# Kernel tuning notes

Measured on AMD Instinct MI355X. Metric: run time of the kernel, lower is better.

The kernel has to match this reference:

```python
import jax, jax.numpy as jnp
import numpy as np

BATCH, SEQ, CHANNELS, KSIZE = 4, 4096, 2048, 4


def setup_inputs() -> dict:
    key = jax.random.key(0)
    kx, kw = jax.random.split(key)
    x = jax.random.normal(kx, (BATCH, SEQ, CHANNELS), dtype=jnp.float32)
    # flax param init: normal(stddev=0.02), shape (kernel_size, channels)
    kernel = jax.random.normal(kw, (KSIZE, CHANNELS), dtype=jnp.float32) * 0.02
    return {"x": x, "kernel": kernel}


def reference(x, kernel):
    # Causal depthwise short conv: y[:, t] = silu(sum_j kernel[j] * x[:, t - j])
    # (the scan's window * kernel[::-1] unrolls to exactly this), with zero
    # left-padding of K-1 steps standing in for cache=None -> zeros.
    B, T, C = x.shape
    K = kernel.shape[0]
    kf = kernel.astype(x.dtype)
    cache = jnp.zeros((B, K - 1, C), dtype=x.dtype)
    xp = jnp.concatenate([cache, x], axis=1)  # [B, T+K-1, C]
    # Small fixed loop over kernel taps (K=4), fully parallel over time.
    y = kf[0][None, None, :] * xp[:, K - 1 : K - 1 + T, :]
    for j in range(1, K):
        y = y + kf[j][None, None, :] * xp[:, K - 1 - j : K - 1 - j + T, :]
    y = jax.nn.silu(y)
    # next_cache after the scan = last K-1 inputs of the padded stream
    next_cache = xp[:, T:, :]  # [B, K-1, C]
    return y, next_cache
```

## Files before the change

kernel.cpp:

```cpp
#include <hip/hip_runtime.h>
#include <math.h>


#define B_   4
#define T_   4096
#define C_   2048
#define K_   4
#define C4_  (C_ / 4)
#define TT_  32

__global__ __launch_bounds__(C4_) void dwconv_silu_kernel(
    const float4* __restrict__ x,
    const float4* __restrict__ kern,
    float4* __restrict__ y)
{
    const int c4 = threadIdx.x;
    const int b  = blockIdx.y;
    const int t0 = blockIdx.x * TT_;

    const float4 k0 = kern[0 * C4_ + c4];
    const float4 k1 = kern[1 * C4_ + c4];
    const float4 k2 = kern[2 * C4_ + c4];
    const float4 k3 = kern[3 * C4_ + c4];

    const float4* xb = x + (size_t)b * T_ * C4_;
    float4*       yb = y + (size_t)b * T_ * C4_;

    float4 xm1, xm2, xm3;
    if (t0 == 0) {
        xm1 = make_float4(0.f, 0.f, 0.f, 0.f);
        xm2 = xm1;
        xm3 = xm1;
    } else {
        xm1 = xb[(size_t)(t0 - 1) * C4_ + c4];
        xm2 = xb[(size_t)(t0 - 2) * C4_ + c4];
        xm3 = xb[(size_t)(t0 - 3) * C4_ + c4];
    }

    #pragma unroll 4
    for (int i = 0; i < TT_; ++i) {
        const int t = t0 + i;
        const float4 x0 = xb[(size_t)t * C4_ + c4];

        float4 r;
        r.x = fmaf(k0.x, x0.x, fmaf(k1.x, xm1.x, fmaf(k2.x, xm2.x, k3.x * xm3.x)));
        r.y = fmaf(k0.y, x0.y, fmaf(k1.y, xm1.y, fmaf(k2.y, xm2.y, k3.y * xm3.y)));
        r.z = fmaf(k0.z, x0.z, fmaf(k1.z, xm1.z, fmaf(k2.z, xm2.z, k3.z * xm3.z)));
        r.w = fmaf(k0.w, x0.w, fmaf(k1.w, xm1.w, fmaf(k2.w, xm2.w, k3.w * xm3.w)));

        r.x = r.x / (1.f + expf(-r.x));
        r.y = r.y / (1.f + expf(-r.y));
        r.z = r.z / (1.f + expf(-r.z));
        r.w = r.w / (1.f + expf(-r.w));

        yb[(size_t)t * C4_ + c4] = r;

        xm3 = xm2;
        xm2 = xm1;
        xm1 = x0;
    }
}

__global__ __launch_bounds__(256) void cache_copy_kernel(
    const float4* __restrict__ x, float4* __restrict__ cache)
{
    const int i = blockIdx.x * blockDim.x + threadIdx.x;
    if (i >= B_ * (K_ - 1) * C4_) return;
    const int b  = i / ((K_ - 1) * C4_);
    const int rc = i % ((K_ - 1) * C4_);
    const int t  = T_ - (K_ - 1) + rc / C4_;
    const int c4 = rc % C4_;
    cache[i] = x[((size_t)b * T_ + t) * C4_ + c4];
}

extern "C" void kernel_launch(void* const* d_in, const int* in_sizes, int n_in,
                              void* d_out, int out_size, void* d_ws, size_t ws_size,
                              hipStream_t stream)
{
    const float4* x    = (const float4*)d_in[0];
    const float4* kern = (const float4*)d_in[1];
    float*        out  = (float*)d_out;

    float4* y     = (float4*)out;
    float4* cache = (float4*)(out + (size_t)B_ * T_ * C_);

    dim3 grid(T_ / TT_, B_);
    dim3 block(C4_);
    dwconv_silu_kernel<<<grid, block, 0, stream>>>(x, kern, y);

    const int cache_elems4 = B_ * (K_ - 1) * C4_;
    cache_copy_kernel<<<(cache_elems4 + 255) / 256, 256, 0, stream>>>(x, cache);
}
```

Before: 242.6 us.

## Unroll conv loop with batched loads, nontemporal stores, fast SiLU, smaller time tile

Halves the per-block time tile, which doubles the block count and adds more halo re-reads. The time loop is fully unrolled so four consecutive rows are loaded together before computing. Output is written with nontemporal stores to avoid polluting cache, and SiLU now uses fast __expf plus a reciprocal instead of a divide. An occupancy hint of 8 blocks per CU is also added to the launch bounds. The intent is more memory-level parallelism for a bandwidth-bound kernel, at a small cost in accuracy from the fast math.

```diff
diff --git a/kernel.cpp b/kernel.cpp
--- a/kernel.cpp
+++ b/kernel.cpp
@@ -7,9 +7,20 @@
 #define C_   2048
 #define K_   4
 #define C4_  (C_ / 4)
-#define TT_  32
+#define TT_  16
 
-__global__ __launch_bounds__(C4_) void dwconv_silu_kernel(
+typedef float nat_float4 __attribute__((ext_vector_type(4)));
+
+__device__ __forceinline__ float silu_f(float v) {
+    return v * __frcp_rn(1.f + __expf(-v));
+}
+
+__device__ __forceinline__ void store_nt(float4* p, const float4& v) {
+    nat_float4 nv = { v.x, v.y, v.z, v.w };
+    __builtin_nontemporal_store(nv, reinterpret_cast<nat_float4*>(p));
+}
+
+__global__ __launch_bounds__(C4_, 8) void dwconv_silu_kernel(
     const float4* __restrict__ x,
     const float4* __restrict__ kern,
     float4* __restrict__ y)
@@ -23,8 +34,8 @@
     const float4 k2 = kern[2 * C4_ + c4];
     const float4 k3 = kern[3 * C4_ + c4];
 
-    const float4* xb = x + (size_t)b * T_ * C4_;
-    float4*       yb = y + (size_t)b * T_ * C4_;
+    const float4* xb = x + (size_t)b * T_ * C4_ + c4;
+    float4*       yb = y + (size_t)b * T_ * C4_ + c4;
 
     float4 xm1, xm2, xm3;
     if (t0 == 0) {
@@ -32,33 +43,41 @@
         xm2 = xm1;
         xm3 = xm1;
     } else {
-        xm1 = xb[(size_t)(t0 - 1) * C4_ + c4];
-        xm2 = xb[(size_t)(t0 - 2) * C4_ + c4];
-        xm3 = xb[(size_t)(t0 - 3) * C4_ + c4];
+        xm1 = xb[(size_t)(t0 - 1) * C4_];
+        xm2 = xb[(size_t)(t0 - 2) * C4_];
+        xm3 = xb[(size_t)(t0 - 3) * C4_];
     }
 
-    #pragma unroll 4
-    for (int i = 0; i < TT_; ++i) {
-        const int t = t0 + i;
-        const float4 x0 = xb[(size_t)t * C4_ + c4];
+#define CONV1(r, a, w1, w2, w3)                                              \
+    r.x = fmaf(k0.x, a.x, fmaf(k1.x, w1.x, fmaf(k2.x, w2.x, k3.x * w3.x)));  \
+    r.y = fmaf(k0.y, a.y, fmaf(k1.y, w1.y, fmaf(k2.y, w2.y, k3.y * w3.y)));  \
+    r.z = fmaf(k0.z, a.z, fmaf(k1.z, w1.z, fmaf(k2.z, w2.z, k3.z * w3.z)));  \
+    r.w = fmaf(k0.w, a.w, fmaf(k1.w, w1.w, fmaf(k2.w, w2.w, k3.w * w3.w)));  \
+    r.x = silu_f(r.x); r.y = silu_f(r.y); r.z = silu_f(r.z); r.w = silu_f(r.w);
 
-        float4 r;
-        r.x = fmaf(k0.x, x0.x, fmaf(k1.x, xm1.x, fmaf(k2.x, xm2.x, k3.x * xm3.x)));
-        r.y = fmaf(k0.y, x0.y, fmaf(k1.y, xm1.y, fmaf(k2.y, xm2.y, k3.y * xm3.y)));
-        r.z = fmaf(k0.z, x0.z, fmaf(k1.z, xm1.z, fmaf(k2.z, xm2.z, k3.z * xm3.z)));
-        r.w = fmaf(k0.w, x0.w, fmaf(k1.w, xm1.w, fmaf(k2.w, xm2.w, k3.w * xm3.w)));
+    #pragma unroll
+    for (int i = 0; i < TT_; i += 4) {
+        const float4 a0 = xb[(size_t)(t0 + i + 0) * C4_];
+        const float4 a1 = xb[(size_t)(t0 + i + 1) * C4_];
+        const float4 a2 = xb[(size_t)(t0 + i + 2) * C4_];
+        const float4 a3 = xb[(size_t)(t0 + i + 3) * C4_];
 
-        r.x = r.x / (1.f + expf(-r.x));
-        r.y = r.y / (1.f + expf(-r.y));
-        r.z = r.z / (1.f + expf(-r.z));
-        r.w = r.w / (1.f + expf(-r.w));
+        float4 r0, r1, r2, r3;
+        CONV1(r0, a0, xm1, xm2, xm3)
+        CONV1(r1, a1, a0,  xm1, xm2)
+        CONV1(r2, a2, a1,  a0,  xm1)
+        CONV1(r3, a3, a2,  a1,  a0)
 
-        yb[(size_t)t * C4_ + c4] = r;
+        store_nt(&yb[(size_t)(t0 + i + 0) * C4_], r0);
+        store_nt(&yb[(size_t)(t0 + i + 1) * C4_], r1);
+        store_nt(&yb[(size_t)(t0 + i + 2) * C4_], r2);
+        store_nt(&yb[(size_t)(t0 + i + 3) * C4_], r3);
 
-        xm3 = xm2;
-        xm2 = xm1;
-        xm1 = x0;
+        xm3 = a1;
+        xm2 = a2;
+        xm1 = a3;
     }
+#undef CONV1
 }
 
 __global__ __launch_bounds__(256) void cache_copy_kernel(
```

New measurement: 238.7 us. Within noise of the previous version (-1.6%).
